# Kernel optimization log

Hardware: AMD Instinct MI355X
Metric: run time of the kernel (lower is better)

## Reference

```python
import jax, jax.numpy as jnp
import numpy as np

N, E = 50000, 800000
IN, HID, OUT = 128, 32, 8


def setup_inputs() -> dict:
    key = jax.random.key(0)
    ks = jax.random.split(key, 20)
    f32 = jnp.float32
    def rn(k, shape, s=0.1):
        return (jax.random.normal(k, shape, dtype=f32) * s)
    return {
        'x': jax.random.normal(ks[0], (N, IN), dtype=f32),
        'edge_index': jax.random.randint(ks[1], (2, E), 0, N, dtype=jnp.int32),
        'edge_attr': jax.random.uniform(ks[2], (E, 1), dtype=f32),
        # layer 1: heads=4, out=HID, concat -> 4*HID channels
        'w1l': rn(ks[3], (IN, 4 * HID)), 'b1l': rn(ks[4], (4 * HID,)),
        'w1r': rn(ks[5], (IN, 4 * HID)), 'b1r': rn(ks[6], (4 * HID,)),
        'w1e': rn(ks[7], (1, 4 * HID)),
        'att1': rn(ks[8], (4, HID)), 'bias1': rn(ks[9], (4 * HID,)),
        # layer 2: heads=2, out=HID, mean over heads -> HID channels
        'w2l': rn(ks[10], (4 * HID, 2 * HID)), 'b2l': rn(ks[11], (2 * HID,)),
        'w2r': rn(ks[12], (4 * HID, 2 * HID)), 'b2r': rn(ks[13], (2 * HID,)),
        'w2e': rn(ks[14], (1, 2 * HID)),
        'att2': rn(ks[15], (2, HID)), 'bias2': rn(ks[16], (HID,)),
        'wc': rn(ks[17], (HID, OUT)), 'bc': rn(ks[18], (OUT,)),
    }


def _add_self_loops(edge_index, edge_attr, n):
    # PyG GATv2Conv adds self-loops; edge feature for loops = mean of edge_attr
    loop = jnp.arange(n, dtype=edge_index.dtype)
    src = jnp.concatenate([edge_index[0], loop])
    dst = jnp.concatenate([edge_index[1], loop])
    mean_attr = jnp.broadcast_to(edge_attr.mean(axis=0), (n, edge_attr.shape[1]))
    ea = jnp.concatenate([edge_attr, mean_attr], axis=0)
    return src, dst, ea


def _gatv2(x, src, dst, eattr, Wl, bl, Wr, br, We, att, bias, heads, out, concat):
    n = x.shape[0]
    xl = (x @ Wl + bl).reshape(n, heads, out)   # source transform (messages)
    xr = (x @ Wr + br).reshape(n, heads, out)   # target transform
    e = (eattr @ We).reshape(-1, heads, out)    # edge embedding
    z = jax.nn.leaky_relu(xl[src] + xr[dst] + e, negative_slope=0.2)  # [Etot,H,D]
    score = jnp.einsum('ehd,hd->eh', z, att)
    # segment softmax over incoming edges of each destination node
    smax = jax.ops.segment_max(score, dst, num_segments=n)
    ex = jnp.exp(score - smax[dst])
    denom = jax.ops.segment_sum(ex, dst, num_segments=n)
    alpha = ex / denom[dst]                     # [Etot,H]
    agg = jax.ops.segment_sum(xl[src] * alpha[..., None], dst, num_segments=n)
    o = agg.reshape(n, heads * out) if concat else agg.mean(axis=1)
    return o + bias


def reference(x, edge_index, edge_attr, w1l, b1l, w1r, b1r, w1e, att1, bias1,
              w2l, b2l, w2r, b2r, w2e, att2, bias2, wc, bc):
    src, dst, ea = _add_self_loops(edge_index, edge_attr, x.shape[0])
    h = _gatv2(x, src, dst, ea, w1l, b1l, w1r, b1r, w1e, att1, bias1, 4, HID, True)
    h = jax.nn.elu(h)
    # dropout p=0.4 is training-only; reference is eval mode (identity)
    h = _gatv2(h, src, dst, ea, w2l, b2l, w2r, b2r, w2e, att2, bias2, 2, HID, False)
    h = jax.nn.elu(h)
    return h @ wc + bc
```

## Files before the change

### kernel.cpp

```cpp
#include <hip/hip_runtime.h>
#include <hip/hip_fp16.h>
#include <math.h>

typedef _Float16 h2_t __attribute__((ext_vector_type(2)));
typedef _Float16 h4_t __attribute__((ext_vector_type(4)));
typedef _Float16 h8_t __attribute__((ext_vector_type(8)));
typedef float f4_t __attribute__((ext_vector_type(4)));
typedef float f8_t __attribute__((ext_vector_type(8)));

#define PRE_BLOCKS 512
#define SB 512
#define NBUK_PAD 800

__device__ inline h8_t load8f_to_h8(const float* p) {
    float4 a = *(const float4*)p;
    float4 b = *(const float4*)(p + 4);
    h8_t r;
    r[0] = (_Float16)a.x; r[1] = (_Float16)a.y; r[2] = (_Float16)a.z; r[3] = (_Float16)a.w;
    r[4] = (_Float16)b.x; r[5] = (_Float16)b.y; r[6] = (_Float16)b.z; r[7] = (_Float16)b.w;
    return r;
}

__device__ inline h4_t load4f_to_h4(const float* p) {
    float4 a = *(const float4*)p;
    h4_t r;
    r[0] = (_Float16)a.x; r[1] = (_Float16)a.y; r[2] = (_Float16)a.z; r[3] = (_Float16)a.w;
    return r;
}

__device__ inline float dot8h(h8_t a, h8_t b, float s) {
    s = __builtin_amdgcn_fdot2(__builtin_shufflevector(a, a, 0, 1),
                               __builtin_shufflevector(b, b, 0, 1), s, false);
    s = __builtin_amdgcn_fdot2(__builtin_shufflevector(a, a, 2, 3),
                               __builtin_shufflevector(b, b, 2, 3), s, false);
    s = __builtin_amdgcn_fdot2(__builtin_shufflevector(a, a, 4, 5),
                               __builtin_shufflevector(b, b, 4, 5), s, false);
    s = __builtin_amdgcn_fdot2(__builtin_shufflevector(a, a, 6, 7),
                               __builtin_shufflevector(b, b, 6, 7), s, false);
    return s;
}

__device__ inline float dot4h(h4_t a, h4_t b, float s) {
    s = __builtin_amdgcn_fdot2(__builtin_shufflevector(a, a, 0, 1),
                               __builtin_shufflevector(b, b, 0, 1), s, false);
    s = __builtin_amdgcn_fdot2(__builtin_shufflevector(a, a, 2, 3),
                               __builtin_shufflevector(b, b, 2, 3), s, false);
    return s;
}

__device__ inline float elu1(float v) { return v > 0.f ? v : __expf(v) - 1.f; }

struct MA {
    const float* x;
    const float* eattr;
    const int* ei;
    const float *w1l, *b1l, *w1r, *b1r, *w1e, *att1, *bias1;
    const float *w2l, *b2l, *w2r, *b2r, *w2e, *att2, *bias2;
    const float *wc, *bc;
    float* out;
    _Float16 *xh, *xl1h, *xr1h, *h1h, *xl2h, *xr2h;
    _Float16 *p1l, *p1r, *p2l, *p2r;
    int *deg, *offb;
    unsigned* parth;
    unsigned *tstart, *tot;
    unsigned* smeanq;
    unsigned* tmp;
    unsigned* flags;
    float* part;
    unsigned* edges;
    int N, E, NW, NBK, CE;
    float invE;
};


__device__ inline void phase_packw(const MA& a, int g) {
    const float* W;
    _Float16* P;
    int M, lg;
    if (g < 2048)      { W = a.w1l; P = a.p1l; M = 128; lg = g; }
    else if (g < 4096) { W = a.w1r; P = a.p1r; M = 128; lg = g - 2048; }
    else if (g < 5120) { W = a.w2l; P = a.p2l; M = 64;  lg = g - 4096; }
    else               { W = a.w2r; P = a.p2r; M = 64;  lg = g - 5120; }
    int ln = lg & 63;
    int s = (lg >> 6) & 3;
    int tt = lg >> 8;
    int m = ln & 15, quad = ln >> 4;
    h8_t v;
#pragma unroll
    for (int j = 0; j < 8; ++j)
        v[j] = (_Float16)W[(size_t)(s * 32 + quad * 8 + j) * M + tt * 16 + m];
    *(h8_t*)(P + (size_t)lg * 8) = v;
}

template <int NT>
__device__ inline void phase_mm_tile(const MA& a, const _Float16* X, int rt, int lane,
                                     const _Float16* Pl, const float* bl, _Float16* Yl,
                                     const _Float16* Pr, const float* br, _Float16* Yr) {
    int nrow = lane & 15, quad = lane >> 4;
    int row = rt * 16 + nrow;
    if (row >= a.N) return;
    const _Float16* xp = X + (size_t)row * 128 + quad * 8;
    h8_t bf0 = *(const h8_t*)(xp);
    h8_t bf1 = *(const h8_t*)(xp + 32);
    h8_t bf2 = *(const h8_t*)(xp + 64);
    h8_t bf3 = *(const h8_t*)(xp + 96);
#pragma unroll
    for (int w = 0; w < 2; ++w) {
        const _Float16* P = w ? Pr : Pl;
        const float* bias = w ? br : bl;
        _Float16* Y = w ? Yr : Yl;
#pragma unroll
        for (int t2 = 0; t2 < NT; ++t2) {
            f4_t acc = {0.f, 0.f, 0.f, 0.f};
            const _Float16* pb = P + (size_t)t2 * 2048 + (size_t)lane * 8;
            acc = __builtin_amdgcn_mfma_f32_16x16x32_f16(*(const h8_t*)pb, bf0, acc, 0, 0, 0);
            acc = __builtin_amdgcn_mfma_f32_16x16x32_f16(*(const h8_t*)(pb + 512), bf1, acc, 0, 0, 0);
            acc = __builtin_amdgcn_mfma_f32_16x16x32_f16(*(const h8_t*)(pb + 1024), bf2, acc, 0, 0, 0);
            acc = __builtin_amdgcn_mfma_f32_16x16x32_f16(*(const h8_t*)(pb + 1536), bf3, acc, 0, 0, 0);
            float4 bv = *(const float4*)(bias + t2 * 16 + quad * 4);
            h4_t o;
            o[0] = (_Float16)(acc[0] + bv.x);
            o[1] = (_Float16)(acc[1] + bv.y);
            o[2] = (_Float16)(acc[2] + bv.z);
            o[3] = (_Float16)(acc[3] + bv.w);
            *(h4_t*)(Y + (size_t)row * (NT * 16) + t2 * 16 + quad * 4) = o;
        }
    }
}


__global__ __launch_bounds__(256) void k_pre(MA a) {
    if (blockIdx.x >= PRE_BLOCKS) {
        int g = (blockIdx.x - PRE_BLOCKS) * 256 + threadIdx.x;
        if (g < 6144) phase_packw(a, g);
        return;
    }
    __shared__ unsigned bh[NBUK_PAD];
    __shared__ float sd[4];
    int tx = threadIdx.x;
    for (int j = tx; j < NBUK_PAD; j += 256) bh[j] = 0u;

    int t = blockIdx.x * 256 + tx;
    const int stride = PRE_BLOCKS * 256;
    for (int i = t; i < NBUK_PAD; i += stride) a.flags[i] = 0u;
    int nchunk = (a.N * 128) >> 3;
    for (int i = t; i < nchunk; i += stride) {
        h8_t v = load8f_to_h8(a.x + (size_t)i * 8);
        *(h8_t*)(a.xh + (size_t)i * 8) = v;
    }
    float s = 0.f;
    for (int i = t; i < a.E; i += stride) s += a.eattr[i];
    for (int o = 1; o < 64; o <<= 1) s += __shfl_xor(s, o, 64);
    if ((tx & 63) == 0) sd[tx >> 6] = s;
    __syncthreads();
    if (tx == 0) a.part[blockIdx.x] = sd[0] + sd[1] + sd[2] + sd[3];

    int e0 = blockIdx.x * a.CE, e1 = min(e0 + a.CE, a.E);
    for (int e = e0 + tx; e < e1; e += 256)
        atomicAdd(&bh[((unsigned)a.ei[a.E + e]) >> 6], 1u);
    __syncthreads();
    for (int j = tx; j < NBUK_PAD; j += 256)
        a.parth[(size_t)blockIdx.x * NBUK_PAD + j] = bh[j];
}


__global__ __launch_bounds__(512, 1) void k_colscan(MA a) {
    __shared__ unsigned lds[512];
    __shared__ unsigned sbase;
    __shared__ float sd[8];
    int tx = threadIdx.x;
    int b = blockIdx.x;
    unsigned v = a.parth[(size_t)tx * NBUK_PAD + b];
    lds[tx] = v;
    __syncthreads();
    for (int o = 1; o < 512; o <<= 1) {
        unsigned u = (tx >= o) ? lds[tx - o] : 0u;
        __syncthreads();
        lds[tx] += u;
        __syncthreads();
    }
    unsigned T = lds[511];
    unsigned excl = lds[tx] - v;
    if (tx == 0) {
        unsigned run = 0;
        if (b == 0) {
            atomicExch(&a.flags[0], (2u << 30) | T);
        } else {
            atomicExch(&a.flags[b], (1u << 30) | T);
            int j = b - 1;
            while (true) {
                unsigned f = atomicAdd(&a.flags[j], 0u);
                unsigned st = f >> 30;
                if (st == 0u) continue;
                run += f & 0x3FFFFFFFu;
                if (st == 2u) break;
                --j;
            }
            atomicExch(&a.flags[b], (2u << 30) | (run + T));
        }
        a.tstart[b] = run;
        a.tot[b] = T;
        sbase = run;
    }
    __syncthreads();
    a.parth[(size_t)tx * NBUK_PAD + b] = sbase + excl;

    if (b == 0) {
        float s = a.part[tx];
        for (int o = 1; o < 64; o <<= 1) s += __shfl_xor(s, o, 64);
        if ((tx & 63) == 0) sd[tx >> 6] = s;
        __syncthreads();
        if (tx == 0) {
            float m = 0.f;
#pragma unroll
            for (int k = 0; k < 8; ++k) m += sd[k];
            a.smeanq[0] = (unsigned)__float2int_rn(m * a.invE * 255.f);
        }
    }
}


__global__ __launch_bounds__(256) void k_scatter(MA a) {
    int bid = blockIdx.x;
    if (bid < a.NW) {
        int wid = bid * 4 + (threadIdx.x >> 6);
        int ntile = (a.N + 15) / 16;
        if (wid < ntile)
            phase_mm_tile<8>(a, a.xh, wid, threadIdx.x & 63,
                             a.p1l, a.b1l, a.xl1h, a.p1r, a.b1r, a.xr1h);
        return;
    }
    __shared__ unsigned cur[NBUK_PAD];
    int s = bid - a.NW;
    int tx = threadIdx.x;
    for (int j = tx; j < NBUK_PAD; j += 256)
        cur[j] = a.parth[(size_t)s * NBUK_PAD + j];
    __syncthreads();
    int e0 = s * a.CE, e1 = min(e0 + a.CE, a.E);
    for (int e = e0 + tx; e < e1; e += 256) {
        int d = a.ei[a.E + e];
        unsigned src = (unsigned)a.ei[e];
        unsigned q = (unsigned)__float2int_rn(a.eattr[e] * 255.f);
        unsigned pos = atomicAdd(&cur[d >> 6], 1u);
        a.tmp[pos] = src | (q << 16) | ((unsigned)(d & 63) << 24);
    }
}


__global__ __launch_bounds__(256) void k_fine(MA a) {
    __shared__ int hist[64];
    __shared__ unsigned cur[64];
    __shared__ unsigned sm;
    int b = blockIdx.x;
    int tx = threadIdx.x;
    int n0 = b << 6;
    int nn = min(64, a.N - n0);
    unsigned ts = a.tstart[b], T = a.tot[b];
    if (tx < 64) hist[tx] = 0;
    if (tx == 0) sm = a.smeanq[0];
    __syncthreads();
    for (unsigned i = tx; i < T; i += 256) {
        unsigned v = a.tmp[ts + i];
        atomicAdd(&hist[(int)(v >> 24)], 1);
    }
    __syncthreads();
    if (tx < 64) {
        int deg1 = hist[tx] + 1;
        int vsc = deg1;
#pragma unroll
        for (int o = 1; o < 64; o <<= 1) {
            int u = __shfl_up(vsc, o, 64);
            if (tx >= o) vsc += u;
        }
        int off = (int)ts + n0 + (vsc - deg1);
        if (tx < nn) {
            a.offb[n0 + tx] = off;
            a.deg[n0 + tx] = deg1;
            a.edges[off] = (unsigned)(n0 + tx) | (sm << 24);
        }
        cur[tx] = (unsigned)(off + 1);
    }
    __syncthreads();
    for (unsigned i = tx; i < T; i += 256) {
        unsigned v = a.tmp[ts + i];
        int loc = (int)(v >> 24);
        unsigned pos = atomicAdd(&cur[loc], 1u);
        a.edges[pos] = (v & 0xFFFFu) | (((v >> 16) & 0xFFu) << 24);
    }
}


__global__ __launch_bounds__(256) void k_node1(MA a) {
    int tid = threadIdx.x;
    int q = tid & 15;
    int node = blockIdx.x * 16 + (tid >> 4);
    if (node >= a.N) return;
    unsigned cb = (unsigned)(q * 16);

    h8_t xrv = *(const h8_t*)((const char*)a.xr1h + ((unsigned)node << 8) + cb);
    h8_t wev = load8f_to_h8(a.w1e + q * 8);
    h8_t atv = load8f_to_h8(a.att1 + q * 8);
    const unsigned* ep = a.edges + a.offb[node];
    int deg1 = a.deg[node];
    int last = deg1 - 1;
    const char* xb = (const char*)a.xl1h;

    float l = 0.f;
    f8_t acc = {0.f, 0.f, 0.f, 0.f, 0.f, 0.f, 0.f, 0.f};

    auto GA = [&](unsigned p) -> h8_t {
        return *(const h8_t*)(xb + (((p & 0x00FFFFFFu) << 8) | cb));
    };
    auto LOADG = [&](int i, unsigned& p0, unsigned& p1, unsigned& p2, unsigned& p3,
                     h8_t& x0, h8_t& x1, h8_t& x2, h8_t& x3) {
        p0 = ep[i];
        p1 = ep[min(i + 1, last)];
        p2 = ep[min(i + 2, last)];
        p3 = ep[min(i + 3, last)];
        x0 = GA(p0); x1 = GA(p1); x2 = GA(p2); x3 = GA(p3);
    };
    auto COMPG = [&](int i, unsigned p0, unsigned p1, unsigned p2, unsigned p3,
                     h8_t x0, h8_t x1, h8_t x2, h8_t x3) {
        float e0 = (float)(p0 >> 24) * (1.f / 255.f);
        float e1 = (float)(p1 >> 24) * (1.f / 255.f);
        float e2 = (float)(p2 >> 24) * (1.f / 255.f);
        float e3 = (float)(p3 >> 24) * (1.f / 255.f);
        h8_t z0 = x0 + xrv + wev * (_Float16)e0;
        z0 = __builtin_elementwise_max(z0, z0 * (_Float16)0.2f);
        float sc0 = dot8h(z0, atv, 0.f);
        h8_t z1 = x1 + xrv + wev * (_Float16)e1;
        z1 = __builtin_elementwise_max(z1, z1 * (_Float16)0.2f);
        float sc1 = dot8h(z1, atv, 0.f);
        h8_t z2 = x2 + xrv + wev * (_Float16)e2;
        z2 = __builtin_elementwise_max(z2, z2 * (_Float16)0.2f);
        float sc2 = dot8h(z2, atv, 0.f);
        h8_t z3 = x3 + xrv + wev * (_Float16)e3;
        z3 = __builtin_elementwise_max(z3, z3 * (_Float16)0.2f);
        float sc3 = dot8h(z3, atv, 0.f);
        sc0 += __shfl_xor(sc0, 1, 64); sc0 += __shfl_xor(sc0, 2, 64);
        sc1 += __shfl_xor(sc1, 1, 64); sc1 += __shfl_xor(sc1, 2, 64);
        sc2 += __shfl_xor(sc2, 1, 64); sc2 += __shfl_xor(sc2, 2, 64);
        sc3 += __shfl_xor(sc3, 1, 64); sc3 += __shfl_xor(sc3, 2, 64);
        float pA = __expf(fminf(sc0, 60.f));
        float pB = (i + 1 < deg1) ? __expf(fminf(sc1, 60.f)) : 0.f;
        float pC = (i + 2 < deg1) ? __expf(fminf(sc2, 60.f)) : 0.f;
        float pD = (i + 3 < deg1) ? __expf(fminf(sc3, 60.f)) : 0.f;
        l += (pA + pB) + (pC + pD);
#pragma unroll
        for (int k = 0; k < 8; ++k)
            acc[k] = fmaf(pA, (float)x0[k],
                     fmaf(pB, (float)x1[k],
                     fmaf(pC, (float)x2[k], fmaf(pD, (float)x3[k], acc[k]))));
    };

    unsigned pa0, pa1, pa2, pa3, pb0, pb1, pb2, pb3;
    h8_t xa0, xa1, xa2, xa3, xb0, xb1, xb2, xb3;
    LOADG(0, pa0, pa1, pa2, pa3, xa0, xa1, xa2, xa3);
    for (int i = 0; i < deg1; i += 8) {
        if (i + 4 < deg1) LOADG(i + 4, pb0, pb1, pb2, pb3, xb0, xb1, xb2, xb3);
        COMPG(i, pa0, pa1, pa2, pa3, xa0, xa1, xa2, xa3);
        if (i + 8 < deg1) LOADG(i + 8, pa0, pa1, pa2, pa3, xa0, xa1, xa2, xa3);
        if (i + 4 < deg1) COMPG(i + 4, pb0, pb1, pb2, pb3, xb0, xb1, xb2, xb3);
    }

    float inv = 1.f / l;
    float4 b0 = *(const float4*)(a.bias1 + q * 8);
    float4 b1 = *(const float4*)(a.bias1 + q * 8 + 4);
    float bb[8] = {b0.x, b0.y, b0.z, b0.w, b1.x, b1.y, b1.z, b1.w};
    h8_t o;
#pragma unroll
    for (int k = 0; k < 8; ++k) o[k] = (_Float16)elu1(fmaf(acc[k], inv, bb[k]));
    *(h8_t*)((char*)a.h1h + ((unsigned)node << 8) + cb) = o;
}


__global__ __launch_bounds__(256) void k_mm4(MA a) {
    int wid = blockIdx.x * 4 + (threadIdx.x >> 6);
    int ntile = (a.N + 15) / 16;
    if (wid >= ntile) return;
    phase_mm_tile<4>(a, a.h1h, wid, threadIdx.x & 63,
                     a.p2l, a.b2l, a.xl2h, a.p2r, a.b2r, a.xr2h);
}


__global__ __launch_bounds__(256) void k_node2(MA a) {
    __shared__ float h2s[16][33];
    int tid = threadIdx.x;
    int lane = tid & 63;
    int wib = tid >> 6;
    int sub = lane >> 4;
    int r = lane & 15;
    int nloc = wib * 4 + sub;
    int node = blockIdx.x * 16 + nloc;
    int c0 = r * 4;

    if (node < a.N) {
        h4_t xrv = *(const h4_t*)(a.xr2h + (size_t)node * 64 + c0);
        h4_t wev = load4f_to_h4(a.w2e + c0);
        h4_t atv = load4f_to_h4(a.att2 + c0);
        const unsigned* ep = a.edges + a.offb[node];
        int deg1 = a.deg[node];
        int last = deg1 - 1;
        const char* xb = (const char*)a.xl2h;
        unsigned cb = (unsigned)(c0 * 2);
        float l = 0.f;
        float acc[4] = {0.f, 0.f, 0.f, 0.f};

        auto GA = [&](unsigned p) -> h4_t {
            return *(const h4_t*)(xb + (((p & 0x00FFFFFFu) << 7) | cb));
        };
        auto LOADG = [&](int i, unsigned& p0, unsigned& p1, unsigned& p2, unsigned& p3,
                         h4_t& x0, h4_t& x1, h4_t& x2, h4_t& x3) {
            p0 = ep[i];
            p1 = ep[min(i + 1, last)];
            p2 = ep[min(i + 2, last)];
            p3 = ep[min(i + 3, last)];
            x0 = GA(p0); x1 = GA(p1); x2 = GA(p2); x3 = GA(p3);
        };
        auto CEDGE = [&](int idx, unsigned p, h4_t xv) {
            float ea = (float)(p >> 24) * (1.f / 255.f);
            h4_t z = xv + xrv + wev * (_Float16)ea;
            z = __builtin_elementwise_max(z, z * (_Float16)0.2f);
            float sc = dot4h(z, atv, 0.f);
            sc += __shfl_xor(sc, 1, 64);
            sc += __shfl_xor(sc, 2, 64);
            sc += __shfl_xor(sc, 4, 64);
            float pp = (idx < deg1) ? __expf(fminf(sc, 60.f)) : 0.f;
            l += pp;
#pragma unroll
            for (int k = 0; k < 4; ++k) acc[k] = fmaf(pp, (float)xv[k], acc[k]);
        };

        unsigned pa0, pa1, pa2, pa3, pb0, pb1, pb2, pb3;
        h4_t xa0, xa1, xa2, xa3, xb0, xb1, xb2, xb3;
        LOADG(0, pa0, pa1, pa2, pa3, xa0, xa1, xa2, xa3);
        for (int i = 0; i < deg1; i += 8) {
            if (i + 4 < deg1) LOADG(i + 4, pb0, pb1, pb2, pb3, xb0, xb1, xb2, xb3);
            CEDGE(i, pa0, xa0); CEDGE(i + 1, pa1, xa1);
            CEDGE(i + 2, pa2, xa2); CEDGE(i + 3, pa3, xa3);
            if (i + 8 < deg1) LOADG(i + 8, pa0, pa1, pa2, pa3, xa0, xa1, xa2, xa3);
            if (i + 4 < deg1) {
                CEDGE(i + 4, pb0, xb0); CEDGE(i + 5, pb1, xb1);
                CEDGE(i + 6, pb2, xb2); CEDGE(i + 7, pb3, xb3);
            }
        }

        float inv = 1.f / l;
#pragma unroll
        for (int k = 0; k < 4; ++k) {
            float norm = acc[k] * inv;
            float other = __shfl_xor(norm, 8, 64);
            float v = 0.5f * (norm + other);
            if (r < 8) h2s[nloc][c0 + k] = elu1(v + a.bias2[c0 + k]);
        }
    }
    __syncthreads();
    if (tid < 128) {
        int n = tid >> 3, j = tid & 7;
        int gnode = blockIdx.x * 16 + n;
        if (gnode < a.N) {
            float acc = a.bc[j];
#pragma unroll 8
            for (int d = 0; d < 32; ++d) acc = fmaf(h2s[n][d], a.wc[d * 8 + j], acc);
            a.out[(size_t)gnode * 8 + j] = acc;
        }
    }
}


extern "C" void kernel_launch(void* const* d_in, const int* in_sizes, int n_in,
                              void* d_out, int out_size, void* d_ws, size_t ws_size,
                              hipStream_t stream) {
    const int N = in_sizes[0] / 128;
    const int E = in_sizes[2];
    const int tot = E + N;

    char* ws = (char*)d_ws;
    size_t o = 0;
    auto alloc = [&](size_t bytes) -> void* {
        void* p = ws + o;
        o += (bytes + 255) & ~(size_t)255;
        return p;
    };
    MA a;
    a.x     = (const float*)d_in[0];
    a.ei    = (const int*)d_in[1];
    a.eattr = (const float*)d_in[2];
    a.w1l = (const float*)d_in[3];  a.b1l = (const float*)d_in[4];
    a.w1r = (const float*)d_in[5];  a.b1r = (const float*)d_in[6];
    a.w1e = (const float*)d_in[7];  a.att1 = (const float*)d_in[8];
    a.bias1 = (const float*)d_in[9];
    a.w2l = (const float*)d_in[10]; a.b2l = (const float*)d_in[11];
    a.w2r = (const float*)d_in[12]; a.b2r = (const float*)d_in[13];
    a.w2e = (const float*)d_in[14]; a.att2 = (const float*)d_in[15];
    a.bias2 = (const float*)d_in[16];
    a.wc = (const float*)d_in[17];  a.bc = (const float*)d_in[18];
    a.out = (float*)d_out;

    a.xh   = (_Float16*)alloc((size_t)N * 128 * 2);
    a.xl1h = (_Float16*)alloc((size_t)N * 128 * 2);
    a.xr1h = (_Float16*)alloc((size_t)N * 128 * 2);
    a.h1h  = (_Float16*)alloc((size_t)N * 128 * 2);
    a.xl2h = (_Float16*)alloc((size_t)N * 64 * 2);
    a.xr2h = (_Float16*)alloc((size_t)N * 64 * 2);
    a.p1l  = (_Float16*)alloc(128 * 128 * 2);
    a.p1r  = (_Float16*)alloc(128 * 128 * 2);
    a.p2l  = (_Float16*)alloc(128 * 64 * 2);
    a.p2r  = (_Float16*)alloc(128 * 64 * 2);
    a.deg  = (int*)alloc((size_t)N * 4);
    a.offb = (int*)alloc((size_t)N * 4);
    a.parth  = (unsigned*)alloc((size_t)SB * NBUK_PAD * 4);
    a.tstart = (unsigned*)alloc(NBUK_PAD * 4);
    a.tot    = (unsigned*)alloc(NBUK_PAD * 4);
    a.smeanq = (unsigned*)alloc(256);
    a.flags  = (unsigned*)alloc(1024 * 4);
    a.part   = (float*)alloc(PRE_BLOCKS * 4);
    a.tmp    = (unsigned*)alloc((size_t)E * 4);
    a.edges  = (unsigned*)alloc((size_t)tot * 4);
    a.N = N;
    a.E = E;
    a.NW = (N + 63) / 64;
    a.NBK = (N + 63) >> 6;
    a.CE = (E + SB - 1) / SB;
    a.invE = 1.0f / (float)E;

    k_pre<<<PRE_BLOCKS + 24, 256, 0, stream>>>(a);
    k_colscan<<<a.NBK, 512, 0, stream>>>(a);
    k_scatter<<<a.NW + SB, 256, 0, stream>>>(a);
    k_fine<<<a.NBK, 256, 0, stream>>>(a);
    k_node1<<<(N + 15) / 16, 256, 0, stream>>>(a);
    k_mm4<<<(N + 63) / 64, 256, 0, stream>>>(a);
    k_node2<<<(N + 15) / 16, 256, 0, stream>>>(a);
}
```

Before: 265.1 us.

## Replace decoupled-lookback bucket scan with separate single-block scan kernel; simplify node2 loop

The cross-block decoupled lookback scan in k_colscan, which spin-waits on global flags, is replaced by a plain per-column scan plus a new one-block k_scan2 kernel. That kernel scans the bucket totals and reduces the edge-attribute mean. k_scatter now adds the bucket base offset when it loads its cursors. The layer-2 node loop drops the double-buffered 8-edge software prefetch in favour of a simpler 4-edge unrolled loop. This removes serialized lookback spinning but adds one kernel launch, and the simpler loop may expose more gather latency.

```diff
diff --git a/kernel.cpp b/kernel.cpp
--- a/kernel.cpp
+++ b/kernel.cpp
@@ -65,7 +65,6 @@
     unsigned *tstart, *tot;
     unsigned* smeanq;
     unsigned* tmp;
-    unsigned* flags;
     float* part;
     unsigned* edges;
     int N, E, NW, NBK, CE;
@@ -142,7 +141,6 @@
 
     int t = blockIdx.x * 256 + tx;
     const int stride = PRE_BLOCKS * 256;
-    for (int i = t; i < NBUK_PAD; i += stride) a.flags[i] = 0u;
     int nchunk = (a.N * 128) >> 3;
     for (int i = t; i < nchunk; i += stride) {
         h8_t v = load8f_to_h8(a.x + (size_t)i * 8);
@@ -166,8 +164,6 @@
 
 __global__ __launch_bounds__(512, 1) void k_colscan(MA a) {
     __shared__ unsigned lds[512];
-    __shared__ unsigned sbase;
-    __shared__ float sd[8];
     int tx = threadIdx.x;
     int b = blockIdx.x;
     unsigned v = a.parth[(size_t)tx * NBUK_PAD + b];
@@ -179,43 +175,33 @@
         lds[tx] += u;
         __syncthreads();
     }
-    unsigned T = lds[511];
-    unsigned excl = lds[tx] - v;
+    a.parth[(size_t)tx * NBUK_PAD + b] = lds[tx] - v;
+    if (tx == 511) a.tot[b] = lds[511];
+}
+
+
+__global__ __launch_bounds__(1024, 1) void k_scan2(MA a) {
+    __shared__ unsigned lds[1024];
+    __shared__ float sd[16];
+    int tx = threadIdx.x;
+    unsigned v = (tx < a.NBK) ? a.tot[tx] : 0u;
+    lds[tx] = v;
+    float s = (tx < PRE_BLOCKS) ? a.part[tx] : 0.f;
+    for (int o = 1; o < 64; o <<= 1) s += __shfl_xor(s, o, 64);
+    if ((tx & 63) == 0) sd[tx >> 6] = s;
+    __syncthreads();
+    for (int o = 1; o < 1024; o <<= 1) {
+        unsigned u = (tx >= o) ? lds[tx - o] : 0u;
+        __syncthreads();
+        lds[tx] += u;
+        __syncthreads();
+    }
+    if (tx < a.NBK) a.tstart[tx] = lds[tx] - v;
     if (tx == 0) {
-        unsigned run = 0;
-        if (b == 0) {
-            atomicExch(&a.flags[0], (2u << 30) | T);
-        } else {
-            atomicExch(&a.flags[b], (1u << 30) | T);
-            int j = b - 1;
-            while (true) {
-                unsigned f = atomicAdd(&a.flags[j], 0u);
-                unsigned st = f >> 30;
-                if (st == 0u) continue;
-                run += f & 0x3FFFFFFFu;
-                if (st == 2u) break;
-                --j;
-            }
-            atomicExch(&a.flags[b], (2u << 30) | (run + T));
-        }
-        a.tstart[b] = run;
-        a.tot[b] = T;
-        sbase = run;
-    }
-    __syncthreads();
-    a.parth[(size_t)tx * NBUK_PAD + b] = sbase + excl;
-
-    if (b == 0) {
-        float s = a.part[tx];
-        for (int o = 1; o < 64; o <<= 1) s += __shfl_xor(s, o, 64);
-        if ((tx & 63) == 0) sd[tx >> 6] = s;
-        __syncthreads();
-        if (tx == 0) {
-            float m = 0.f;
-#pragma unroll
-            for (int k = 0; k < 8; ++k) m += sd[k];
-            a.smeanq[0] = (unsigned)__float2int_rn(m * a.invE * 255.f);
-        }
+        float m = 0.f;
+#pragma unroll
+        for (int k = 0; k < 16; ++k) m += sd[k];
+        a.smeanq[0] = (unsigned)__float2int_rn(m * a.invE * 255.f);
     }
 }
 
@@ -234,7 +220,7 @@
     int s = bid - a.NW;
     int tx = threadIdx.x;
     for (int j = tx; j < NBUK_PAD; j += 256)
-        cur[j] = a.parth[(size_t)s * NBUK_PAD + j];
+        cur[j] = a.parth[(size_t)s * NBUK_PAD + j] + a.tstart[j];
     __syncthreads();
     int e0 = s * a.CE, e1 = min(e0 + a.CE, a.E);
     for (int e = e0 + tx; e < e1; e += 256) {
@@ -405,46 +391,29 @@
         unsigned cb = (unsigned)(c0 * 2);
         float l = 0.f;
         float acc[4] = {0.f, 0.f, 0.f, 0.f};
-
-        auto GA = [&](unsigned p) -> h4_t {
-            return *(const h4_t*)(xb + (((p & 0x00FFFFFFu) << 7) | cb));
-        };
-        auto LOADG = [&](int i, unsigned& p0, unsigned& p1, unsigned& p2, unsigned& p3,
-                         h4_t& x0, h4_t& x1, h4_t& x2, h4_t& x3) {
-            p0 = ep[i];
-            p1 = ep[min(i + 1, last)];
-            p2 = ep[min(i + 2, last)];
-            p3 = ep[min(i + 3, last)];
-            x0 = GA(p0); x1 = GA(p1); x2 = GA(p2); x3 = GA(p3);
-        };
-        auto CEDGE = [&](int idx, unsigned p, h4_t xv) {
-            float ea = (float)(p >> 24) * (1.f / 255.f);
-            h4_t z = xv + xrv + wev * (_Float16)ea;
-            z = __builtin_elementwise_max(z, z * (_Float16)0.2f);
-            float sc = dot4h(z, atv, 0.f);
-            sc += __shfl_xor(sc, 1, 64);
-            sc += __shfl_xor(sc, 2, 64);
-            sc += __shfl_xor(sc, 4, 64);
-            float pp = (idx < deg1) ? __expf(fminf(sc, 60.f)) : 0.f;
-            l += pp;
-#pragma unroll
-            for (int k = 0; k < 4; ++k) acc[k] = fmaf(pp, (float)xv[k], acc[k]);
-        };
-
-        unsigned pa0, pa1, pa2, pa3, pb0, pb1, pb2, pb3;
-        h4_t xa0, xa1, xa2, xa3, xb0, xb1, xb2, xb3;
-        LOADG(0, pa0, pa1, pa2, pa3, xa0, xa1, xa2, xa3);
-        for (int i = 0; i < deg1; i += 8) {
-            if (i + 4 < deg1) LOADG(i + 4, pb0, pb1, pb2, pb3, xb0, xb1, xb2, xb3);
-            CEDGE(i, pa0, xa0); CEDGE(i + 1, pa1, xa1);
-            CEDGE(i + 2, pa2, xa2); CEDGE(i + 3, pa3, xa3);
-            if (i + 8 < deg1) LOADG(i + 8, pa0, pa1, pa2, pa3, xa0, xa1, xa2, xa3);
-            if (i + 4 < deg1) {
-                CEDGE(i + 4, pb0, xb0); CEDGE(i + 5, pb1, xb1);
-                CEDGE(i + 6, pb2, xb2); CEDGE(i + 7, pb3, xb3);
+        for (int i = 0; i < deg1; i += 4) {
+            unsigned p[4];
+            h4_t xv[4];
+#pragma unroll
+            for (int j = 0; j < 4; ++j) p[j] = ep[min(i + j, last)];
+#pragma unroll
+            for (int j = 0; j < 4; ++j)
+                xv[j] = *(const h4_t*)(xb + (((p[j] & 0x00FFFFFFu) << 7) | cb));
+#pragma unroll
+            for (int j = 0; j < 4; ++j) {
+                float ea = (float)(p[j] >> 24) * (1.f / 255.f);
+                h4_t z = xv[j] + xrv + wev * (_Float16)ea;
+                z = __builtin_elementwise_max(z, z * (_Float16)0.2f);
+                float sc = dot4h(z, atv, 0.f);
+                sc += __shfl_xor(sc, 1, 64);
+                sc += __shfl_xor(sc, 2, 64);
+                sc += __shfl_xor(sc, 4, 64);
+                float pp = (i + j < deg1) ? __expf(fminf(sc, 60.f)) : 0.f;
+                l += pp;
+#pragma unroll
+                for (int k = 0; k < 4; ++k) acc[k] = fmaf(pp, (float)xv[j][k], acc[k]);
             }
         }
-
         float inv = 1.f / l;
 #pragma unroll
         for (int k = 0; k < 4; ++k) {
@@ -510,10 +479,9 @@
     a.deg  = (int*)alloc((size_t)N * 4);
     a.offb = (int*)alloc((size_t)N * 4);
     a.parth  = (unsigned*)alloc((size_t)SB * NBUK_PAD * 4);
-    a.tstart = (unsigned*)alloc(NBUK_PAD * 4);
-    a.tot    = (unsigned*)alloc(NBUK_PAD * 4);
+    a.tstart = (unsigned*)alloc(1024 * 4);
+    a.tot    = (unsigned*)alloc(1024 * 4);
     a.smeanq = (unsigned*)alloc(256);
-    a.flags  = (unsigned*)alloc(1024 * 4);
     a.part   = (float*)alloc(PRE_BLOCKS * 4);
     a.tmp    = (unsigned*)alloc((size_t)E * 4);
     a.edges  = (unsigned*)alloc((size_t)tot * 4);
@@ -526,6 +494,7 @@
 
     k_pre<<<PRE_BLOCKS + 24, 256, 0, stream>>>(a);
     k_colscan<<<a.NBK, 512, 0, stream>>>(a);
+    k_scan2<<<1, 1024, 0, stream>>>(a);
     k_scatter<<<a.NW + SB, 256, 0, stream>>>(a);
     k_fine<<<a.NBK, 256, 0, stream>>>(a);
     k_node1<<<(N + 15) / 16, 256, 0, stream>>>(a);
```

Measured after the change: 239.3 us. -9.7%, faster.
